# Kernel optimization log

Hardware: AMD Instinct MI355X
Metric: run time of the kernel (lower is better)

The kernel has to match this reference:

```python
import itertools
import jax, jax.numpy as jnp
import numpy as np


def _interpn_linear(vol, loc):
    """Trilinear sampling with edge-clamping (voxelmorph interpn, fill_value=None).
    vol: [D, H, W, C] float; loc: [D, H, W, 3] float absolute sample coordinates (ij indexing).
    """
    spatial = vol.shape[:-1]
    ndims = len(spatial)
    maxs = jnp.asarray([s - 1 for s in spatial], dtype=loc.dtype)
    cloc = jnp.clip(loc, 0.0, maxs)             # clamp = nearest-neighbor fill outside domain
    loc0 = jnp.floor(cloc)
    loc1 = jnp.minimum(loc0 + 1.0, maxs)
    d1 = loc1 - cloc                            # weight for the low corner (loc0)
    d0 = 1.0 - d1                               # weight for the high corner (loc1)
    loc0i = loc0.astype(jnp.int32)
    loc1i = loc1.astype(jnp.int32)

    # flatten volume and build per-dim strides for linear indexing
    volf = vol.reshape(-1, vol.shape[-1])       # [D*H*W, C]
    strides = np.ones(ndims, dtype=np.int32)
    for d in range(ndims - 2, -1, -1):
        strides[d] = strides[d + 1] * spatial[d + 1]

    out = jnp.zeros(spatial + (vol.shape[-1],), dtype=vol.dtype)
    for corner in itertools.product((0, 1), repeat=ndims):
        idx = jnp.zeros(spatial, dtype=jnp.int32)
        w = jnp.ones(spatial, dtype=vol.dtype)
        for d in range(ndims):
            idx = idx + (loc1i if corner[d] else loc0i)[..., d] * strides[d]
            w = w * (d0 if corner[d] else d1)[..., d]
        out = out + w[..., None] * jnp.take(volf, idx, axis=0)
    return out


def _warp_single(vol, disp):
    """Apply dense displacement field: sample vol at identity grid + disp."""
    spatial = vol.shape[:-1]
    grid = jnp.stack(
        jnp.meshgrid(*[jnp.arange(s, dtype=disp.dtype) for s in spatial], indexing='ij'),
        axis=-1)                                # [D, H, W, 3]
    return _interpn_linear(vol, grid + disp)


def setup_inputs() -> dict:
    key = jax.random.key(0)
    k1, k2 = jax.random.split(key)
    vol = jax.random.normal(k1, (2, 128, 192, 192, 1), dtype=jnp.float32)
    trf = jax.random.normal(k2, (2, 128, 192, 192, 3), dtype=jnp.float32)
    return {"vol": vol, "trf": trf}


def reference(vol, trf):
    # batched dense-warp spatial transformer (single_transform=False)
    return jax.vmap(_warp_single)(vol, trf)
```

## Files before the change

### kernel.cpp

```cpp
#include <hip/hip_runtime.h>
#include <stdint.h>


#define BD 128
#define BH 192
#define BW 192
#define DHW (BD*BH*BW)
#define NB 2

#define TX 16
#define TY 8
#define NTX (BW/TX)
#define NTY (BH/TY)
#define ZSTEP 4
#define NSTEPB 8
#define BLKZ (ZSTEP*NSTEPB)
#define NZB (BD/BLKZ)
#define NBLK (NTX*NTY*NZB*NB)
#define NXCD 8

#define SXW 32
#define SYW 16
#define SLAB (SXW*SYW)
#define RING 16
#define LDSF (RING*SLAB)

typedef float f4v __attribute__((ext_vector_type(4)));
typedef float f2v __attribute__((ext_vector_type(2)));

__global__ __launch_bounds__(256, 5) void st_warp_kernel(
    const float* __restrict__ vol,
    const float* __restrict__ trf,
    float* __restrict__ out)
{
    __shared__ __align__(16) float lds[LDSF];

    const int bid = blockIdx.x;
    const int swz = (bid % NXCD) * (NBLK / NXCD) + bid / NXCD;
    int t = swz;
    const int txi = t % NTX; t /= NTX;
    const int tyi = t % NTY; t /= NTY;
    const int kzb = t % NZB; t /= NZB;
    const int b   = t;
    const int tx = txi*TX, ty = tyi*TY;
    const int zA = kzb * BLKZ;

    const int sx = min(max(tx - 8, 0), BW - SXW);
    const int sy = min(max(ty - 4, 0), BH - SYW);

    const int tid = (int)threadIdx.x;
    const float* volb = vol + (size_t)b * DHW;

    const int xp = tid & 7;
    const int yb = (tid >> 3) & 7;
    const int zb = tid >> 6;
    const int Y  = ty + yb;
    const int X0 = tx + xp*2;

    auto stage = [&](int zfirst, int nslab) {
        const int nch = nslab << 7;
        for (int it = 0; it*256 < nch; ++it) {
            const int f = tid + it*256;
            if (f < nch) {
                const int z  = zfirst + (f >> 7);
                const int s  = f & 127;
                const int yi = s >> 3;
                const int c  = s & 7;
                const int slot = z & (RING-1);
                const float* g = volb + ((size_t)(z*BH + sy + yi))*BW + sx + (c<<2);
                __builtin_amdgcn_global_load_lds(
                    (const __attribute__((address_space(1))) void*)g,
                    (__attribute__((address_space(3))) void*)&lds[(slot<<9) + (s<<2)],
                    16, 0, 0);
            }
        }
    };

    const f2v* t2 = (const f2v*)trf;
    auto load_trf = [&](int ZS, f2v& D0, f2v& D1, f2v& D2) {
        const size_t base2 = (((size_t)((b*BD + ZS + zb)*BH + Y))*BW + X0) * 3 / 2;
        D0 = t2[base2 + 0];
        D1 = t2[base2 + 1];
        D2 = t2[base2 + 2];
    };

    auto compute_vals = [&](int ZS, f2v D0, f2v D1, f2v D2) -> f2v {
        const int Z   = ZS + zb;
        const int wlo = max(0, ZS - 4);
        const int whi = min(BD - 1, ZS + 7);
        const float dzs[2] = {D0.x, D1.y};
        const float dys[2] = {D0.y, D2.x};
        const float dxs[2] = {D1.x, D2.y};
        float res[2];
#pragma unroll
        for (int jj = 0; jj < 2; ++jj) {
            float cz = fminf((float)Z + dzs[jj], (float)(BD-1));
            float cy = fminf((float)Y + dys[jj], (float)(BH-1));
            float cx = fminf((float)(X0+jj) + dxs[jj], (float)(BW-1));
            float fz = floorf(cz), fy = floorf(cy), fx = floorf(cx);
            int z0 = (int)fz, y0 = (int)fy, x0 = (int)fx;
            int z1 = min(z0+1, BD-1);
            int y1 = min(y0+1, BH-1);
            int x1 = min(x0+1, BW-1);
            float wz = cz - fz, wy = cy - fy, wx = cx - fx;
            float v000,v001,v010,v011,v100,v101,v110,v111;
            bool inwin = (x0 >= sx) & (x1 <= sx+SXW-1) & (y0 >= sy) & (y1 <= sy+SYW-1)
                       & (z0 >= wlo) & (z1 <= whi);
            if (inwin) {
                const int xi  = x0 - sx;
                const int xiA = min(xi, SXW-2);
                const bool lo = xi < SXW-1;
                const int sl0 = z0 & (RING-1);
                const int sl1 = z1 & (RING-1);
                const int yt0 = (y0 - sy) << 5, yt1 = (y1 - sy) << 5;
                const int rA = (sl0<<9) + yt0 + xiA;
                const int rB = (sl0<<9) + yt1 + xiA;
                const int rC = (sl1<<9) + yt0 + xiA;
                const int rD = (sl1<<9) + yt1 + xiA;
                float a00 = lds[rA], b00 = lds[rA+1];
                float a01 = lds[rB], b01 = lds[rB+1];
                float a10 = lds[rC], b10 = lds[rC+1];
                float a11 = lds[rD], b11 = lds[rD+1];
                v000 = lo ? a00 : b00;  v001 = b00;
                v010 = lo ? a01 : b01;  v011 = b01;
                v100 = lo ? a10 : b10;  v101 = b10;
                v110 = lo ? a11 : b11;  v111 = b11;
            } else {
                const int z0c = max(z0, 0), z1c = max(z1, 0);
                const int y0c = max(y0, 0), y1c = max(y1, 0);
                const int x0c = max(x0, 0), x1c = max(x1, 0);
                const float* p00 = volb + ((size_t)z0c*BH + y0c)*BW;
                const float* p01 = volb + ((size_t)z0c*BH + y1c)*BW;
                const float* p10 = volb + ((size_t)z1c*BH + y0c)*BW;
                const float* p11 = volb + ((size_t)z1c*BH + y1c)*BW;
                v000 = p00[x0c]; v001 = p00[x1c];
                v010 = p01[x0c]; v011 = p01[x1c];
                v100 = p10[x0c]; v101 = p10[x1c];
                v110 = p11[x0c]; v111 = p11[x1c];
            }
            float c00 = v000 + wx*(v001-v000);
            float c01 = v010 + wx*(v011-v010);
            float c10 = v100 + wx*(v101-v100);
            float c11 = v110 + wx*(v111-v110);
            float c0  = c00 + wy*(c01-c00);
            float c1  = c10 + wy*(c11-c10);
            res[jj]   = c0 + wz*(c1-c0);
        }
        f2v r = {res[0], res[1]};
        return r;
    };

    f2v D0[2], D1[2], D2[2];
    stage(max(0, zA - 4), (zA == 0) ? 8 : 12);
    load_trf(zA, D0[0], D1[0], D2[0]);
    __syncthreads();

#pragma unroll
    for (int k = 0; k < NSTEPB; ++k) {
        const int ZS = zA + k*ZSTEP;
        if (k + 1 < NSTEPB) {
            const int zn = ZS + 8;
            if (zn < BD) stage(zn, min(4, BD - zn));
            load_trf(ZS + ZSTEP, D0[(k+1)&1], D1[(k+1)&1], D2[(k+1)&1]);
        }
        f2v r = compute_vals(ZS, D0[k&1], D1[k&1], D2[k&1]);
        const size_t of2 = (((size_t)((b*BD + ZS + zb)*BH + Y))*BW + X0) / 2;
        __builtin_nontemporal_store(r, &((f2v*)out)[of2]);
        __syncthreads();
    }
}

extern "C" void kernel_launch(void* const* d_in, const int* in_sizes, int n_in,
                              void* d_out, int out_size, void* d_ws, size_t ws_size,
                              hipStream_t stream) {
    const float* vol = (const float*)d_in[0];
    const float* trf = (const float*)d_in[1];
    float* out = (float*)d_out;

    st_warp_kernel<<<dim3(NBLK), dim3(256), 0, stream>>>(vol, trf, out);
}
```

Baseline: 44.05 us.

## Deepen LDS slab ring to prefetch two steps ahead with partial vmcnt barriers

```diff
diff --git a/kernel.cpp b/kernel.cpp
--- a/kernel.cpp
+++ b/kernel.cpp
@@ -22,13 +22,28 @@
 #define SXW 32
 #define SYW 16
 #define SLAB (SXW*SYW)
-#define RING 16
+#define RING 20
 #define LDSF (RING*SLAB)
 
 typedef float f4v __attribute__((ext_vector_type(4)));
 typedef float f2v __attribute__((ext_vector_type(2)));
 
-__global__ __launch_bounds__(256, 5) void st_warp_kernel(
+__device__ __forceinline__ int mod20(int z) {
+    return (int)((unsigned)z % 20u);
+}
+
+#define STEP_BARRIER_V6() do {                                         \
+    asm volatile("s_waitcnt vmcnt(6) lgkmcnt(0)" ::: "memory");        \
+    __builtin_amdgcn_s_barrier();                                      \
+    __builtin_amdgcn_sched_barrier(0);                                 \
+} while (0)
+#define STEP_BARRIER_V4() do {                                         \
+    asm volatile("s_waitcnt vmcnt(4) lgkmcnt(0)" ::: "memory");        \
+    __builtin_amdgcn_s_barrier();                                      \
+    __builtin_amdgcn_sched_barrier(0);                                 \
+} while (0)
+
+__global__ __launch_bounds__(256, 4) void st_warp_kernel(
     const float* __restrict__ vol,
     const float* __restrict__ trf,
     float* __restrict__ out)
@@ -58,21 +73,19 @@
     const int X0 = tx + xp*2;
 
     auto stage = [&](int zfirst, int nslab) {
-        const int nch = nslab << 7;
-        for (int it = 0; it*256 < nch; ++it) {
-            const int f = tid + it*256;
-            if (f < nch) {
-                const int z  = zfirst + (f >> 7);
-                const int s  = f & 127;
-                const int yi = s >> 3;
-                const int c  = s & 7;
-                const int slot = z & (RING-1);
-                const float* g = volb + ((size_t)(z*BH + sy + yi))*BW + sx + (c<<2);
-                __builtin_amdgcn_global_load_lds(
-                    (const __attribute__((address_space(1))) void*)g,
-                    (__attribute__((address_space(3))) void*)&lds[(slot<<9) + (s<<2)],
-                    16, 0, 0);
-            }
+        const int iters = nslab >> 1;
+        for (int it = 0; it < iters; ++it) {
+            const int f  = tid + it*256;
+            const int z  = zfirst + (f >> 7);
+            const int s  = f & 127;
+            const int yi = s >> 3;
+            const int c  = s & 7;
+            const int slot = mod20(z);
+            const float* g = volb + ((size_t)(z*BH + sy + yi))*BW + sx + (c<<2);
+            __builtin_amdgcn_global_load_lds(
+                (const __attribute__((address_space(1))) void*)g,
+                (__attribute__((address_space(3))) void*)&lds[(slot<<9) + (s<<2)],
+                16, 0, 0);
         }
     };
 
@@ -110,8 +123,10 @@
                 const int xi  = x0 - sx;
                 const int xiA = min(xi, SXW-2);
                 const bool lo = xi < SXW-1;
-                const int sl0 = z0 & (RING-1);
-                const int sl1 = z1 & (RING-1);
+                const int sl0 = mod20(z0);
+                int sl1 = sl0 + 1;
+                sl1 = (sl1 == RING) ? 0 : sl1;
+                sl1 = (z1 == z0) ? sl0 : sl1;
                 const int yt0 = (y0 - sy) << 5, yt1 = (y1 - sy) << 5;
                 const int rA = (sl0<<9) + yt0 + xiA;
                 const int rB = (sl0<<9) + yt1 + xiA;
@@ -150,23 +165,36 @@
         return r;
     };
 
+    auto store_out = [&](int ZS, f2v r) {
+        const size_t of2 = (((size_t)((b*BD + ZS + zb)*BH + Y))*BW + X0) / 2;
+        __builtin_nontemporal_store(r, &((f2v*)out)[of2]);
+    };
+
     f2v D0[2], D1[2], D2[2];
-    stage(max(0, zA - 4), (zA == 0) ? 8 : 12);
+    stage(max(0, zA - 4), (zA == 0) ? 12 : 16);
     load_trf(zA, D0[0], D1[0], D2[0]);
     __syncthreads();
 
 #pragma unroll
-    for (int k = 0; k < NSTEPB; ++k) {
+    for (int k = 0; k < 6; ++k) {
         const int ZS = zA + k*ZSTEP;
-        if (k + 1 < NSTEPB) {
-            const int zn = ZS + 8;
-            if (zn < BD) stage(zn, min(4, BD - zn));
-            load_trf(ZS + ZSTEP, D0[(k+1)&1], D1[(k+1)&1], D2[(k+1)&1]);
-        }
+        load_trf(ZS + ZSTEP, D0[(k+1)&1], D1[(k+1)&1], D2[(k+1)&1]);
+        stage(min(ZS + 12, BD - 4), 4);
         f2v r = compute_vals(ZS, D0[k&1], D1[k&1], D2[k&1]);
-        const size_t of2 = (((size_t)((b*BD + ZS + zb)*BH + Y))*BW + X0) / 2;
-        __builtin_nontemporal_store(r, &((f2v*)out)[of2]);
-        __syncthreads();
+        store_out(ZS, r);
+        STEP_BARRIER_V6();
+    }
+    {
+        const int ZS = zA + 6*ZSTEP;
+        load_trf(ZS + ZSTEP, D0[1], D1[1], D2[1]);
+        f2v r = compute_vals(ZS, D0[0], D1[0], D2[0]);
+        store_out(ZS, r);
+        STEP_BARRIER_V4();
+    }
+    {
+        const int ZS = zA + 7*ZSTEP;
+        f2v r = compute_vals(ZS, D0[1], D1[1], D2[1]);
+        store_out(ZS, r);
     }
 }
 
```

New measurement: 45.27 us. 2.8% more time.
